# Performance work log

Hardware: AMD Instinct MI355X
Metric: run time of the kernel (lower is better)

Reference implementation:

```python
import math
import jax, jax.numpy as jnp
import numpy as np

B, N, D, O = 8, 2048, 128, 128


def setup_inputs() -> dict:
    key = jax.random.key(0)
    ks = jax.random.split(key, 8)
    s = 1.0 / math.sqrt(D)
    x = jax.random.normal(ks[0], (B, N, D), dtype=jnp.float32)
    A = jax.random.bernoulli(ks[1], 0.02, (B, N, N)).astype(jnp.float32)
    W_qk = jax.random.normal(ks[2], (D, D), dtype=jnp.float32) * s
    b_qk = jnp.zeros((D,), dtype=jnp.float32)
    W_l = jax.random.normal(ks[3], (D, O), dtype=jnp.float32) * s
    b_l = jnp.zeros((O,), dtype=jnp.float32)
    W_r = jax.random.normal(ks[4], (D, O), dtype=jnp.float32) * s
    W_d = jax.random.normal(ks[5], (1, D), dtype=jnp.float32)
    b_d = jnp.zeros((D,), dtype=jnp.float32)
    return {"x": x, "A": A, "W_qk": W_qk, "b_qk": b_qk, "W_l": W_l,
            "b_l": b_l, "W_r": W_r, "W_d": W_d, "b_d": b_d}


def reference(x, A, W_qk, b_qk, W_l, b_l, W_r, W_d, b_d):
    d = x.shape[-1]
    # degree gate: sigmoid(Linear(deg)) scales features
    deg = jnp.sum(A, axis=-1, keepdims=True)              # (B,N,1)
    gate = jax.nn.sigmoid(deg @ W_d + b_d)                # (B,N,D)
    xg = x * gate                                         # (B,N,D)
    # sigmoid QK projection and dense NxN scores
    QK = jax.nn.sigmoid(xg @ W_qk + b_qk)                 # (B,N,D)
    scores = jnp.einsum('bnd,bmd->bnm', QK, QK) / jnp.sqrt(jnp.float32(d))
    scores = scores * A                                   # adjacency mask
    attn = scores / (jnp.sum(scores, axis=-1, keepdims=True) + 1e-6)
    agg = jnp.einsum('bnm,bmd->bnd', attn, xg)            # (B,N,D)
    out = agg @ W_l + b_l + xg @ W_r                      # (B,N,O)
    # F.normalize(p=2, dim=-1): x / max(||x||, eps)
    nrm = jnp.linalg.norm(out, axis=-1, keepdims=True)
    return out / jnp.maximum(nrm, 1e-12)
```

## Files before the change

### kernel.cpp

```cpp
#include <hip/hip_runtime.h>
#include <hip/hip_bf16.h>

#define B_ 8
#define N_ 2048
#define D_ 128
#define NROW (B_*N_)

typedef __bf16 bf16;
typedef __bf16 bf16x8 __attribute__((ext_vector_type(8)));
typedef float f32x4 __attribute__((ext_vector_type(4)));

__device__ __forceinline__ float sigmoidf_(float x) {
    return 1.0f / (1.0f + __expf(-x));
}

__global__ __launch_bounds__(256) void k_wtrans(const float* __restrict__ Wqk,
        const float* __restrict__ Wl, const float* __restrict__ Wr,
        bf16* __restrict__ wqkT, bf16* __restrict__ wlT, bf16* __restrict__ wrT) {
    int m = blockIdx.x >> 3;
    int chunk = blockIdx.x & 7;
    const float* W = (m == 0) ? Wqk : (m == 1 ? Wl : Wr);
    bf16* WT = (m == 0) ? wqkT : (m == 1 ? wlT : wrT);
#pragma unroll
    for (int e = 0; e < 8; ++e) {
        int idx = e * 256 + threadIdx.x;
        int ol = idx >> 7;
        int i  = idx & 127;
        int o = chunk * 16 + ol;
        WT[o * 128 + i] = (bf16)W[i * 128 + o];
    }
}

__global__ __launch_bounds__(256) void k_deg_mask(const float* __restrict__ A,
        unsigned long long* __restrict__ mask, float* __restrict__ deg) {
    const int row = blockIdx.x;
    const float* a = A + (size_t)row * N_;
    const int t = threadIdx.x, w = t >> 6, lane = t & 63;
    __shared__ int partial[4];
    int cnt = 0;
    unsigned long long* mrow = mask + (size_t)row * (N_ / 64);
#pragma unroll
    for (int i = 0; i < N_ / 256; ++i) {
        float v = a[i * 256 + t];
        unsigned long long b = __ballot(v != 0.0f);
        if (lane == 0) { mrow[i * 4 + w] = b; cnt += __popcll(b); }
    }
    if (lane == 0) partial[w] = cnt;
    __syncthreads();
    if (t == 0) deg[row] = (float)(partial[0] + partial[1] + partial[2] + partial[3]);
}

__global__ __launch_bounds__(256) void k_proj(const float* __restrict__ x,
        const float* __restrict__ deg, const float* __restrict__ Wd,
        const float* __restrict__ bd, const bf16* __restrict__ wqkT,
        const float* __restrict__ bqk,
        bf16* __restrict__ qkG, bf16* __restrict__ xgG, bf16* __restrict__ xgTG) {
    __shared__ bf16 wq[128][136];
    __shared__ bf16 xgl[64][136];
    const int t = threadIdx.x, lane = t & 63, w = t >> 6;
    const int rowbase = blockIdx.x * 64;
    {
        int r = t >> 1, h = t & 1;
        const bf16* src = wqkT + r * 128 + h * 64;
#pragma unroll
        for (int k = 0; k < 64; k += 8)
            *(bf16x8*)&wq[r][h * 64 + k] = *(const bf16x8*)(src + k);
    }
#pragma unroll
    for (int e = 0; e < 32; ++e) {
        int idx = e * 256 + t;
        int rl = idx >> 7;
        int d  = idx & 127;
        size_t fr = (size_t)rowbase + rl;
        float g = sigmoidf_(deg[fr] * Wd[d] + bd[d]);
        float v = x[fr * 128 + d] * g;
        bf16 bv = (bf16)v;
        xgl[rl][d] = bv;
        xgG[fr * 128 + d] = bv;
    }
    __syncthreads();
    const int cIdx = lane & 15, g4 = lane >> 4;
    bf16x8 ax[4];
#pragma unroll
    for (int c = 0; c < 4; ++c)
        ax[c] = *(const bf16x8*)&xgl[w * 16 + cIdx][c * 32 + g4 * 8];
#pragma unroll
    for (int dsub = 0; dsub < 8; ++dsub) {
        f32x4 acc = {0.f, 0.f, 0.f, 0.f};
#pragma unroll
        for (int c = 0; c < 4; ++c) {
            bf16x8 bw = *(const bf16x8*)&wq[dsub * 16 + cIdx][c * 32 + g4 * 8];
            acc = __builtin_amdgcn_mfma_f32_16x16x32_bf16(ax[c], bw, acc, 0, 0, 0);
        }
        int col = dsub * 16 + cIdx;
        float bb = bqk[col];
#pragma unroll
        for (int r = 0; r < 4; ++r) {
            size_t row = (size_t)rowbase + w * 16 + g4 * 4 + r;
            qkG[row * 128 + col] = (bf16)sigmoidf_(acc[r] + bb);
        }
    }
    {
        int b = rowbase / N_;
        int nbase = rowbase % N_;
#pragma unroll
        for (int e = 0; e < 32; ++e) {
            int idx = e * 256 + t;
            int d  = idx >> 6;
            int nl = idx & 63;
            xgTG[((size_t)b * 128 + d) * N_ + nbase + nl] = xgl[nl][d];
        }
    }
}

__global__ __launch_bounds__(256) void k_attn(const bf16* __restrict__ qkG,
        const bf16* __restrict__ xgTG, const unsigned long long* __restrict__ maskG,
        bf16* __restrict__ aggG) {
    __shared__ bf16 qkj[128][136];
    __shared__ bf16 xgt[128][136];
    __shared__ bf16 plds[4][16][136];
    __shared__ unsigned long long ml[64][2];
    const int t = threadIdx.x, lane = t & 63, w = t >> 6;
    const int b = blockIdx.x >> 5;
    const int rowbase = (blockIdx.x & 31) * 64;
    const int cIdx = lane & 15, g4 = lane >> 4;
    const int wrow = rowbase + w * 16;
    bf16x8 aq[4];
    {
        const bf16* src = qkG + ((size_t)(b * N_ + wrow + cIdx)) * 128 + g4 * 8;
#pragma unroll
        for (int c = 0; c < 4; ++c) aq[c] = *(const bf16x8*)(src + c * 32);
    }
    f32x4 num[8];
#pragma unroll
    for (int i = 0; i < 8; ++i) num[i] = {0.f, 0.f, 0.f, 0.f};
    float rs[4] = {0.f, 0.f, 0.f, 0.f};
    const float inv = 0.08838834764831845f;
    for (int j = 0; j < N_ / 128; ++j) {
        const int jbase = j * 128;
        __syncthreads();
        {
            int r = t >> 1, h = t & 1;
            const bf16* s1 = qkG + ((size_t)(b * N_ + jbase + r)) * 128 + h * 64;
            const bf16* s2 = xgTG + ((size_t)(b * 128 + r)) * N_ + jbase + h * 64;
#pragma unroll
            for (int k = 0; k < 64; k += 8) {
                *(bf16x8*)&qkj[r][h * 64 + k] = *(const bf16x8*)(s1 + k);
                *(bf16x8*)&xgt[r][h * 64 + k] = *(const bf16x8*)(s2 + k);
            }
            if (t < 128) {
                int rr = t >> 1, ww = t & 1;
                ml[rr][ww] = maskG[((size_t)(b * N_ + rowbase + rr)) * (N_ / 64) + jbase / 64 + ww];
            }
        }
        __syncthreads();
#pragma unroll
        for (int csub = 0; csub < 8; ++csub) {
            f32x4 s = {0.f, 0.f, 0.f, 0.f};
#pragma unroll
            for (int c = 0; c < 4; ++c) {
                bf16x8 bq = *(const bf16x8*)&qkj[csub * 16 + cIdx][c * 32 + g4 * 8];
                s = __builtin_amdgcn_mfma_f32_16x16x32_bf16(aq[c], bq, s, 0, 0, 0);
            }
#pragma unroll
            for (int r = 0; r < 4; ++r) {
                unsigned long long mw = ml[w * 16 + g4 * 4 + r][csub >> 2];
                float v = s[r] * inv;
                int bit = (csub & 3) * 16 + cIdx;
                v = ((mw >> bit) & 1ull) ? v : 0.0f;
                rs[r] += v;
                plds[w][g4 * 4 + r][csub * 16 + cIdx] = (bf16)v;
            }
        }
        __syncthreads();
        bf16x8 ap[4];
#pragma unroll
        for (int c = 0; c < 4; ++c)
            ap[c] = *(const bf16x8*)&plds[w][cIdx][c * 32 + g4 * 8];
#pragma unroll
        for (int dsub = 0; dsub < 8; ++dsub) {
#pragma unroll
            for (int c = 0; c < 4; ++c) {
                bf16x8 bx = *(const bf16x8*)&xgt[dsub * 16 + cIdx][c * 32 + g4 * 8];
                num[dsub] = __builtin_amdgcn_mfma_f32_16x16x32_bf16(ap[c], bx, num[dsub], 0, 0, 0);
            }
        }
    }
#pragma unroll
    for (int r = 0; r < 4; ++r) {
        rs[r] += __shfl_xor(rs[r], 1, 64);
        rs[r] += __shfl_xor(rs[r], 2, 64);
        rs[r] += __shfl_xor(rs[r], 4, 64);
        rs[r] += __shfl_xor(rs[r], 8, 64);
    }
    float sc[4];
#pragma unroll
    for (int r = 0; r < 4; ++r) sc[r] = 1.0f / (rs[r] + 1e-6f);
#pragma unroll
    for (int dsub = 0; dsub < 8; ++dsub)
#pragma unroll
        for (int r = 0; r < 4; ++r) {
            size_t row = (size_t)b * N_ + wrow + g4 * 4 + r;
            aggG[row * 128 + dsub * 16 + cIdx] = (bf16)(num[dsub][r] * sc[r]);
        }
}

__global__ __launch_bounds__(256) void k_out(const bf16* __restrict__ aggG,
        const bf16* __restrict__ xgG, const bf16* __restrict__ wlT,
        const bf16* __restrict__ wrT, const float* __restrict__ blv,
        float* __restrict__ out) {
    __shared__ bf16 wl[128][136];
    __shared__ bf16 wr[128][136];
    __shared__ bf16 ag[64][136];
    __shared__ bf16 xgl[64][136];
    const int t = threadIdx.x, lane = t & 63, w = t >> 6;
    const int rowbase = blockIdx.x * 64;
    {
        int r = t >> 1, h = t & 1;
#pragma unroll
        for (int k = 0; k < 64; k += 8) {
            *(bf16x8*)&wl[r][h * 64 + k] = *(const bf16x8*)(wlT + r * 128 + h * 64 + k);
            *(bf16x8*)&wr[r][h * 64 + k] = *(const bf16x8*)(wrT + r * 128 + h * 64 + k);
        }
        int rl = t >> 2, q = t & 3;
        const bf16* s1 = aggG + ((size_t)(rowbase + rl)) * 128 + q * 32;
        const bf16* s2 = xgG + ((size_t)(rowbase + rl)) * 128 + q * 32;
#pragma unroll
        for (int k = 0; k < 32; k += 8) {
            *(bf16x8*)&ag[rl][q * 32 + k] = *(const bf16x8*)(s1 + k);
            *(bf16x8*)&xgl[rl][q * 32 + k] = *(const bf16x8*)(s2 + k);
        }
    }
    __syncthreads();
    const int cIdx = lane & 15, g4 = lane >> 4;
    bf16x8 aa[4], ax[4];
#pragma unroll
    for (int c = 0; c < 4; ++c) {
        aa[c] = *(const bf16x8*)&ag[w * 16 + cIdx][c * 32 + g4 * 8];
        ax[c] = *(const bf16x8*)&xgl[w * 16 + cIdx][c * 32 + g4 * 8];
    }
    f32x4 acc[8];
    float ss[4] = {0.f, 0.f, 0.f, 0.f};
#pragma unroll
    for (int osub = 0; osub < 8; ++osub) {
        float bb = blv[osub * 16 + cIdx];
        f32x4 a = {bb, bb, bb, bb};
#pragma unroll
        for (int c = 0; c < 4; ++c) {
            bf16x8 b1 = *(const bf16x8*)&wl[osub * 16 + cIdx][c * 32 + g4 * 8];
            a = __builtin_amdgcn_mfma_f32_16x16x32_bf16(aa[c], b1, a, 0, 0, 0);
            bf16x8 b2 = *(const bf16x8*)&wr[osub * 16 + cIdx][c * 32 + g4 * 8];
            a = __builtin_amdgcn_mfma_f32_16x16x32_bf16(ax[c], b2, a, 0, 0, 0);
        }
        acc[osub] = a;
#pragma unroll
        for (int r = 0; r < 4; ++r) ss[r] += a[r] * a[r];
    }
#pragma unroll
    for (int r = 0; r < 4; ++r) {
        ss[r] += __shfl_xor(ss[r], 1, 64);
        ss[r] += __shfl_xor(ss[r], 2, 64);
        ss[r] += __shfl_xor(ss[r], 4, 64);
        ss[r] += __shfl_xor(ss[r], 8, 64);
    }
    float sc[4];
#pragma unroll
    for (int r = 0; r < 4; ++r) sc[r] = 1.0f / fmaxf(sqrtf(ss[r]), 1e-12f);
#pragma unroll
    for (int osub = 0; osub < 8; ++osub)
#pragma unroll
        for (int r = 0; r < 4; ++r) {
            size_t row = (size_t)rowbase + w * 16 + g4 * 4 + r;
            out[row * 128 + osub * 16 + cIdx] = acc[osub][r] * sc[r];
        }
}

extern "C" void kernel_launch(void* const* d_in, const int* in_sizes, int n_in,
                              void* d_out, int out_size, void* d_ws, size_t ws_size,
                              hipStream_t stream) {
    const float* x   = (const float*)d_in[0];
    const float* A   = (const float*)d_in[1];
    const float* Wqk = (const float*)d_in[2];
    const float* bqk = (const float*)d_in[3];
    const float* Wl  = (const float*)d_in[4];
    const float* bl  = (const float*)d_in[5];
    const float* Wr  = (const float*)d_in[6];
    const float* Wd  = (const float*)d_in[7];
    const float* bd  = (const float*)d_in[8];
    float* out = (float*)d_out;
    char* ws = (char*)d_ws;

    unsigned long long* maskG = (unsigned long long*)ws;
    float* degG = (float*)(ws + (4 << 20));
    bf16* wqkT  = (bf16*)(ws + (5 << 20));
    bf16* wlT   = (bf16*)(ws + (5 << 20) + 32768);
    bf16* wrT   = (bf16*)(ws + (5 << 20) + 65536);
    bf16* qkG   = (bf16*)(ws + (6 << 20));
    bf16* xgG   = (bf16*)(ws + (10 << 20));
    bf16* xgTG  = (bf16*)(ws + (14 << 20));
    bf16* aggG  = (bf16*)(ws + (18 << 20));

    hipLaunchKernelGGL(k_wtrans, dim3(24), dim3(256), 0, stream, Wqk, Wl, Wr, wqkT, wlT, wrT);
    hipLaunchKernelGGL(k_deg_mask, dim3(NROW), dim3(256), 0, stream, A, maskG, degG);
    hipLaunchKernelGGL(k_proj, dim3(NROW / 64), dim3(256), 0, stream,
                       x, degG, Wd, bd, wqkT, bqk, qkG, xgG, xgTG);
    hipLaunchKernelGGL(k_attn, dim3(NROW / 64), dim3(256), 0, stream, qkG, xgTG, maskG, aggG);
    hipLaunchKernelGGL(k_out, dim3(NROW / 64), dim3(256), 0, stream, aggG, xgG, wlT, wrT, bl, out);
}
```

Baseline: 305.0 us.

## Restructure attention kernel with split-K waves, async LDS double buffering, swizzled layout

Rewrites the attention kernel to use 512 threads, with waves split across four key-range quarters and two row halves. Each stage is double-buffered in LDS through global_load_lds direct-to-LDS copies into XOR-swizzled tiles, which overlaps loads with MFMA work and avoids bank conflicts. The partial numerators and row sums are reduced through LDS at the end. The degree/mask kernel now uses float4 loads with 32-bit mask words. The cost is a 145KB LDS footprint, which may limit occupancy, plus an extra cross-quarter reduction pass.

```diff
diff --git a/kernel.cpp b/kernel.cpp
--- a/kernel.cpp
+++ b/kernel.cpp
@@ -12,6 +12,12 @@
 
 __device__ __forceinline__ float sigmoidf_(float x) {
     return 1.0f / (1.0f + __expf(-x));
+}
+
+__device__ __forceinline__ void g2l16(const bf16* g, void* l) {
+    __builtin_amdgcn_global_load_lds(
+        (const __attribute__((address_space(1))) unsigned int*)g,
+        (__attribute__((address_space(3))) unsigned int*)l, 16, 0, 0);
 }
 
 __global__ __launch_bounds__(256) void k_wtrans(const float* __restrict__ Wqk,
@@ -32,19 +38,32 @@
 }
 
 __global__ __launch_bounds__(256) void k_deg_mask(const float* __restrict__ A,
-        unsigned long long* __restrict__ mask, float* __restrict__ deg) {
+        unsigned int* __restrict__ mask, float* __restrict__ deg) {
     const int row = blockIdx.x;
     const float* a = A + (size_t)row * N_;
     const int t = threadIdx.x, w = t >> 6, lane = t & 63;
     __shared__ int partial[4];
     int cnt = 0;
-    unsigned long long* mrow = mask + (size_t)row * (N_ / 64);
-#pragma unroll
-    for (int i = 0; i < N_ / 256; ++i) {
-        float v = a[i * 256 + t];
-        unsigned long long b = __ballot(v != 0.0f);
-        if (lane == 0) { mrow[i * 4 + w] = b; cnt += __popcll(b); }
-    }
+    unsigned int* mrow = mask + (size_t)row * (N_ / 32);
+#pragma unroll
+    for (int i = 0; i < N_ / 1024; ++i) {
+        float4 v = *(const float4*)(a + i * 1024 + t * 4);
+        unsigned long long nib = (unsigned long long)((v.x != 0.f) | ((v.y != 0.f) << 1) |
+                                                      ((v.z != 0.f) << 2) | ((v.w != 0.f) << 3));
+        unsigned long long p = nib << ((t & 15) * 4);
+        p |= __shfl_xor(p, 1);
+        p |= __shfl_xor(p, 2);
+        p |= __shfl_xor(p, 4);
+        p |= __shfl_xor(p, 8);
+        if ((t & 15) == 0) {
+            int idx = i * 32 + (t >> 4) * 2;
+            mrow[idx] = (unsigned int)p;
+            mrow[idx + 1] = (unsigned int)(p >> 32);
+            cnt += __popcll(p);
+        }
+    }
+    cnt += __shfl_xor(cnt, 16);
+    cnt += __shfl_xor(cnt, 32);
     if (lane == 0) partial[w] = cnt;
     __syncthreads();
     if (t == 0) deg[row] = (float)(partial[0] + partial[1] + partial[2] + partial[3]);
@@ -113,96 +132,167 @@
     }
 }
 
-__global__ __launch_bounds__(256) void k_attn(const bf16* __restrict__ qkG,
-        const bf16* __restrict__ xgTG, const unsigned long long* __restrict__ maskG,
+__global__ __launch_bounds__(512, 2) void k_attn(const bf16* __restrict__ qkG,
+        const bf16* __restrict__ xgTG, const unsigned int* __restrict__ mask32,
         bf16* __restrict__ aggG) {
-    __shared__ bf16 qkj[128][136];
-    __shared__ bf16 xgt[128][136];
-    __shared__ bf16 plds[4][16][136];
-    __shared__ unsigned long long ml[64][2];
+    __shared__ __align__(16) char LDSC[148480];
     const int t = threadIdx.x, lane = t & 63, w = t >> 6;
-    const int b = blockIdx.x >> 5;
-    const int rowbase = (blockIdx.x & 31) * 64;
+    const int q = w >> 1, s = w & 1;
     const int cIdx = lane & 15, g4 = lane >> 4;
-    const int wrow = rowbase + w * 16;
-    bf16x8 aq[4];
+    const int bid = (blockIdx.x & 7) * 32 + (blockIdx.x >> 3);
+    const int b = bid >> 5;
+    const int rowbase = (bid & 31) * 64;
+    const int R0 = rowbase + s * 32;
+
+    const int sq = w & 3;
+    const bool stq = (w < 4);
+
+    auto do_stage = [&](int ts, int bbuf) {
+        const int jbase = sq * 512 + ts * 32;
+        if (stq) {
+            const int rowi = lane >> 4;
+            const int g = lane & 15;
+#pragma unroll
+            for (int i = 0; i < 8; ++i) {
+                int row = i * 4 + rowi;
+                const bf16* gsrc = qkG + ((size_t)(b * N_ + jbase + row)) * 128 + ((g ^ (row & 7)) << 3);
+                g2l16(gsrc, LDSC + (bbuf * 4 + sq) * 8192 + i * 1024);
+            }
+        } else {
+            const int di = lane >> 2;
+            const int g = lane & 3;
+#pragma unroll
+            for (int i = 0; i < 8; ++i) {
+                int d = i * 16 + di;
+                const bf16* gsrc = xgTG + ((size_t)(b * 128 + d)) * N_ + jbase + ((g ^ ((d >> 2) & 3)) << 3);
+                g2l16(gsrc, LDSC + 65536 + (bbuf * 4 + sq) * 8192 + i * 1024);
+            }
+        }
+    };
+
+    bf16x8 aq[2][4];
+#pragma unroll
+    for (int isub = 0; isub < 2; ++isub) {
+        const bf16* src = qkG + ((size_t)(b * N_ + R0 + isub * 16 + cIdx)) * 128 + g4 * 8;
+#pragma unroll
+        for (int kc = 0; kc < 4; ++kc) aq[isub][kc] = *(const bf16x8*)(src + kc * 32);
+    }
+    const unsigned int* mrow = mask32 + ((size_t)(b * N_ + R0 + (lane & 31))) * (N_ / 32) + q * 16;
+    unsigned int mw_cur = (lane < 32) ? mrow[0] : 0u;
+
+    do_stage(0, 0);
+    __syncthreads();
+
+    f32x4 num[2][8];
+#pragma unroll
+    for (int i = 0; i < 2; ++i)
+#pragma unroll
+        for (int jd = 0; jd < 8; ++jd) num[i][jd] = {0.f, 0.f, 0.f, 0.f};
+    float rs[2][4] = {{0.f, 0.f, 0.f, 0.f}, {0.f, 0.f, 0.f, 0.f}};
+    const float inv = 0.08838834764831845f;
+
+    for (int ts = 0; ts < 16; ++ts) {
+        const int bb = ts & 1;
+        unsigned int mw_nxt = 0;
+        if (ts < 15) {
+            mw_nxt = (lane < 32) ? mrow[ts + 1] : 0u;
+            do_stage(ts + 1, bb ^ 1);
+        }
+        const char* qb = LDSC + (bb * 4 + q) * 8192;
+        f32x4 sv[2][2];
+#pragma unroll
+        for (int i = 0; i < 2; ++i) { sv[i][0] = {0.f,0.f,0.f,0.f}; sv[i][1] = {0.f,0.f,0.f,0.f}; }
+#pragma unroll
+        for (int kc = 0; kc < 4; ++kc) {
+#pragma unroll
+            for (int csub = 0; csub < 2; ++csub) {
+                int jl = csub * 16 + cIdx;
+                bf16x8 bq = *(const bf16x8*)(qb + jl * 256 + ((((kc << 2) | g4) ^ (jl & 7)) << 4));
+                sv[0][csub] = __builtin_amdgcn_mfma_f32_16x16x32_bf16(aq[0][kc], bq, sv[0][csub], 0, 0, 0);
+                sv[1][csub] = __builtin_amdgcn_mfma_f32_16x16x32_bf16(aq[1][kc], bq, sv[1][csub], 0, 0, 0);
+            }
+        }
+        char* pb = LDSC + 131072 + w * 2048;
+#pragma unroll
+        for (int isub = 0; isub < 2; ++isub)
+#pragma unroll
+        for (int r = 0; r < 4; ++r) {
+            int rl = isub * 16 + g4 * 4 + r;
+            unsigned int mwv = __shfl(mw_cur, rl);
+#pragma unroll
+            for (int csub = 0; csub < 2; ++csub) {
+                float v = sv[isub][csub][r] * inv;
+                v = ((mwv >> (csub * 16 + cIdx)) & 1u) ? v : 0.0f;
+                rs[isub][r] += v;
+                *(bf16*)(pb + rl * 64 + ((((csub << 1) | (cIdx >> 3)) ^ ((rl >> 2) & 3)) << 4)
+                         + ((cIdx & 7) << 1)) = (bf16)v;
+            }
+        }
+        const char* xb = LDSC + 65536 + (bb * 4 + q) * 8192;
+        bf16x8 ap[2];
+#pragma unroll
+        for (int isub = 0; isub < 2; ++isub) {
+            int rl = isub * 16 + cIdx;
+            ap[isub] = *(const bf16x8*)(pb + rl * 64 + ((g4 ^ ((rl >> 2) & 3)) << 4));
+        }
+#pragma unroll
+        for (int dsub = 0; dsub < 8; ++dsub) {
+            int d = dsub * 16 + cIdx;
+            bf16x8 bx = *(const bf16x8*)(xb + d * 64 + ((g4 ^ ((d >> 2) & 3)) << 4));
+            num[0][dsub] = __builtin_amdgcn_mfma_f32_16x16x32_bf16(ap[0], bx, num[0][dsub], 0, 0, 0);
+            num[1][dsub] = __builtin_amdgcn_mfma_f32_16x16x32_bf16(ap[1], bx, num[1][dsub], 0, 0, 0);
+        }
+        mw_cur = mw_nxt;
+        __syncthreads();
+    }
+
+#pragma unroll
+    for (int isub = 0; isub < 2; ++isub)
+#pragma unroll
+    for (int r = 0; r < 4; ++r) {
+        float v = rs[isub][r];
+        v += __shfl_xor(v, 1); v += __shfl_xor(v, 2); v += __shfl_xor(v, 4); v += __shfl_xor(v, 8);
+        rs[isub][r] = v;
+    }
+    float* RSB = (float*)(LDSC + 147456);
+    if (cIdx == 0) {
+#pragma unroll
+        for (int isub = 0; isub < 2; ++isub)
+#pragma unroll
+        for (int r = 0; r < 4; ++r)
+            RSB[(s * 32 + isub * 16 + g4 * 4 + r) * 4 + q] = rs[isub][r];
+    }
+    float* PART = (float*)LDSC;
+#pragma unroll
+    for (int isub = 0; isub < 2; ++isub)
+#pragma unroll
+    for (int dsub = 0; dsub < 8; ++dsub)
+#pragma unroll
+    for (int r = 0; r < 4; ++r)
+        PART[q * 8192 + (s * 32 + isub * 16 + g4 * 4 + r) * 128 + dsub * 16 + cIdx] = num[isub][dsub][r];
+    __syncthreads();
     {
-        const bf16* src = qkG + ((size_t)(b * N_ + wrow + cIdx)) * 128 + g4 * 8;
-#pragma unroll
-        for (int c = 0; c < 4; ++c) aq[c] = *(const bf16x8*)(src + c * 32);
-    }
-    f32x4 num[8];
-#pragma unroll
-    for (int i = 0; i < 8; ++i) num[i] = {0.f, 0.f, 0.f, 0.f};
-    float rs[4] = {0.f, 0.f, 0.f, 0.f};
-    const float inv = 0.08838834764831845f;
-    for (int j = 0; j < N_ / 128; ++j) {
-        const int jbase = j * 128;
-        __syncthreads();
-        {
-            int r = t >> 1, h = t & 1;
-            const bf16* s1 = qkG + ((size_t)(b * N_ + jbase + r)) * 128 + h * 64;
-            const bf16* s2 = xgTG + ((size_t)(b * 128 + r)) * N_ + jbase + h * 64;
-#pragma unroll
-            for (int k = 0; k < 64; k += 8) {
-                *(bf16x8*)&qkj[r][h * 64 + k] = *(const bf16x8*)(s1 + k);
-                *(bf16x8*)&xgt[r][h * 64 + k] = *(const bf16x8*)(s2 + k);
-            }
-            if (t < 128) {
-                int rr = t >> 1, ww = t & 1;
-                ml[rr][ww] = maskG[((size_t)(b * N_ + rowbase + rr)) * (N_ / 64) + jbase / 64 + ww];
-            }
-        }
-        __syncthreads();
-#pragma unroll
-        for (int csub = 0; csub < 8; ++csub) {
-            f32x4 s = {0.f, 0.f, 0.f, 0.f};
-#pragma unroll
-            for (int c = 0; c < 4; ++c) {
-                bf16x8 bq = *(const bf16x8*)&qkj[csub * 16 + cIdx][c * 32 + g4 * 8];
-                s = __builtin_amdgcn_mfma_f32_16x16x32_bf16(aq[c], bq, s, 0, 0, 0);
-            }
-#pragma unroll
-            for (int r = 0; r < 4; ++r) {
-                unsigned long long mw = ml[w * 16 + g4 * 4 + r][csub >> 2];
-                float v = s[r] * inv;
-                int bit = (csub & 3) * 16 + cIdx;
-                v = ((mw >> bit) & 1ull) ? v : 0.0f;
-                rs[r] += v;
-                plds[w][g4 * 4 + r][csub * 16 + cIdx] = (bf16)v;
-            }
-        }
-        __syncthreads();
-        bf16x8 ap[4];
-#pragma unroll
-        for (int c = 0; c < 4; ++c)
-            ap[c] = *(const bf16x8*)&plds[w][cIdx][c * 32 + g4 * 8];
-#pragma unroll
-        for (int dsub = 0; dsub < 8; ++dsub) {
-#pragma unroll
-            for (int c = 0; c < 4; ++c) {
-                bf16x8 bx = *(const bf16x8*)&xgt[dsub * 16 + cIdx][c * 32 + g4 * 8];
-                num[dsub] = __builtin_amdgcn_mfma_f32_16x16x32_bf16(ap[c], bx, num[dsub], 0, 0, 0);
-            }
-        }
-    }
-#pragma unroll
-    for (int r = 0; r < 4; ++r) {
-        rs[r] += __shfl_xor(rs[r], 1, 64);
-        rs[r] += __shfl_xor(rs[r], 2, 64);
-        rs[r] += __shfl_xor(rs[r], 4, 64);
-        rs[r] += __shfl_xor(rs[r], 8, 64);
-    }
-    float sc[4];
-#pragma unroll
-    for (int r = 0; r < 4; ++r) sc[r] = 1.0f / (rs[r] + 1e-6f);
-#pragma unroll
-    for (int dsub = 0; dsub < 8; ++dsub)
-#pragma unroll
-        for (int r = 0; r < 4; ++r) {
-            size_t row = (size_t)b * N_ + wrow + g4 * 4 + r;
-            aggG[row * 128 + dsub * 16 + cIdx] = (bf16)(num[dsub][r] * sc[r]);
-        }
+        int row = t >> 3, colbase = (t & 7) * 16;
+        float accv[16];
+#pragma unroll
+        for (int k = 0; k < 16; ++k) accv[k] = 0.f;
+#pragma unroll
+        for (int q4 = 0; q4 < 4; ++q4)
+#pragma unroll
+            for (int k = 0; k < 4; ++k) {
+                f32x4 pv = *(const f32x4*)(PART + q4 * 8192 + row * 128 + colbase + k * 4);
+                accv[k * 4 + 0] += pv[0]; accv[k * 4 + 1] += pv[1];
+                accv[k * 4 + 2] += pv[2]; accv[k * 4 + 3] += pv[3];
+            }
+        float den = RSB[row * 4 + 0] + RSB[row * 4 + 1] + RSB[row * 4 + 2] + RSB[row * 4 + 3] + 1e-6f;
+        float sc = 1.0f / den;
+        bf16x8 o0, o1;
+#pragma unroll
+        for (int k = 0; k < 8; ++k) { o0[k] = (bf16)(accv[k] * sc); o1[k] = (bf16)(accv[8 + k] * sc); }
+        bf16* dst = aggG + ((size_t)(b * N_ + rowbase + row)) * 128 + colbase;
+        *(bf16x8*)dst = o0;
+        *(bf16x8*)(dst + 8) = o1;
+    }
 }
 
 __global__ __launch_bounds__(256) void k_out(const bf16* __restrict__ aggG,
@@ -258,10 +348,10 @@
     }
 #pragma unroll
     for (int r = 0; r < 4; ++r) {
-        ss[r] += __shfl_xor(ss[r], 1, 64);
-        ss[r] += __shfl_xor(ss[r], 2, 64);
-        ss[r] += __shfl_xor(ss[r], 4, 64);
-        ss[r] += __shfl_xor(ss[r], 8, 64);
+        ss[r] += __shfl_xor(ss[r], 1);
+        ss[r] += __shfl_xor(ss[r], 2);
+        ss[r] += __shfl_xor(ss[r], 4);
+        ss[r] += __shfl_xor(ss[r], 8);
     }
     float sc[4];
 #pragma unroll
@@ -290,7 +380,7 @@
     float* out = (float*)d_out;
     char* ws = (char*)d_ws;
 
-    unsigned long long* maskG = (unsigned long long*)ws;
+    unsigned int* maskG = (unsigned int*)ws;
     float* degG = (float*)(ws + (4 << 20));
     bf16* wqkT  = (bf16*)(ws + (5 << 20));
     bf16* wlT   = (bf16*)(ws + (5 << 20) + 32768);
@@ -304,6 +394,6 @@
     hipLaunchKernelGGL(k_deg_mask, dim3(NROW), dim3(256), 0, stream, A, maskG, degG);
     hipLaunchKernelGGL(k_proj, dim3(NROW / 64), dim3(256), 0, stream,
                        x, degG, Wd, bd, wqkT, bqk, qkG, xgG, xgTG);
-    hipLaunchKernelGGL(k_attn, dim3(NROW / 64), dim3(256), 0, stream, qkG, xgTG, maskG, aggG);
+    hipLaunchKernelGGL(k_attn, dim3(NROW / 64), dim3(512), 0, stream, qkG, xgTG, maskG, aggG);
     hipLaunchKernelGGL(k_out, dim3(NROW / 64), dim3(256), 0, stream, aggG, xgG, wlT, wrT, bl, out);
 }
```

Result: faster. 262.2 us (-14.0%).
